# Kernel tuning notes

Measured on AMD Instinct MI355X. Metric: run time of the kernel, lower is better.

Reference implementation:

```python
import jax, jax.numpy as jnp
import numpy as np

NUM_EXPERTS = 8
TOP_K = 2
HIDDEN = 1024
INTER = 4096
BATCH, SEQ = 4, 2048
AUX_COEF = 0.01
Z_COEF = 0.001


def setup_inputs() -> dict:
    key = jax.random.key(0)
    ks = jax.random.split(key, 5)
    scale = 1.0 / np.sqrt(HIDDEN)
    return {
        "hidden_states": jax.random.normal(ks[0], (BATCH, SEQ, HIDDEN), jnp.float32),
        "gate_w": jax.random.normal(ks[1], (NUM_EXPERTS, HIDDEN), jnp.float32) * scale,
        "w_gate": jax.random.normal(ks[2], (NUM_EXPERTS, INTER, HIDDEN), jnp.float32) * scale,
        "w_up": jax.random.normal(ks[3], (NUM_EXPERTS, INTER, HIDDEN), jnp.float32) * scale,
        "w_down": jax.random.normal(ks[4], (NUM_EXPERTS, HIDDEN, INTER), jnp.float32) * (1.0 / np.sqrt(INTER)),
    }


def reference(hidden_states, gate_w, w_gate, w_up, w_down):
    B, S, H = hidden_states.shape
    x = hidden_states.reshape(-1, H)  # [T, H]
    T = x.shape[0]

    # ---- Router ----
    router_logits = x @ gate_w.T                       # [T, E]
    router_probs = jax.nn.softmax(router_logits, axis=-1)
    routing_weights, selected_experts = jax.lax.top_k(router_probs, TOP_K)  # [T, K]
    routing_weights = routing_weights / routing_weights.sum(axis=-1, keepdims=True)

    # ---- Aux losses ----
    expert_mask = jax.nn.one_hot(selected_experts, NUM_EXPERTS, dtype=jnp.float32).sum(axis=1)  # [T, E]
    tokens_per_expert = expert_mask.mean(axis=0)        # [E]
    prob_per_expert = router_probs.mean(axis=0)         # [E]
    load_balancing_loss = NUM_EXPERTS * (tokens_per_expert * prob_per_expert).sum() * AUX_COEF
    router_z_loss = jnp.mean(jax.nn.logsumexp(router_logits, axis=-1) ** 2) * Z_COEF

    # ---- Combine weights: [T, E], zero for unselected experts ----
    combine = (jax.nn.one_hot(selected_experts, NUM_EXPERTS, dtype=x.dtype)
               * routing_weights[..., None]).sum(axis=1)  # [T, E]

    # ---- Expert SwiGLU FFNs, weighted combine (loop over fixed small E) ----
    out = jnp.zeros_like(x)
    for e in range(NUM_EXPERTS):
        h = jax.nn.silu(x @ w_gate[e].T) * (x @ w_up[e].T)  # [T, INTER]
        out = out + combine[:, e:e + 1] * (h @ w_down[e].T)

    return out.reshape(B, S, H), load_balancing_loss, router_z_loss
```

## Files before the change

kernel.cpp:

```cpp
#include <hip/hip_runtime.h>
#include <hip/hip_bf16.h>

#define NUM_TOK 8192
#define HID 1024
#define INT_DIM 4096
#define NEXP 8
#define NSLOT 16384

typedef __bf16 bf16x8 __attribute__((ext_vector_type(8)));
typedef float f32x4 __attribute__((ext_vector_type(4)));

typedef const __attribute__((address_space(1))) unsigned int* gas_t;
typedef __attribute__((address_space(3))) unsigned int* las_t;

__device__ __forceinline__ void gl_lds16(const unsigned short* g, unsigned short* l) {
    __builtin_amdgcn_global_load_lds((gas_t)g, (las_t)l, 16, 0, 0);
}

__device__ __forceinline__ unsigned short f2bf(float f) {
    unsigned int x = __builtin_bit_cast(unsigned int, f);
    x += 0x7fffu + ((x >> 16) & 1u);
    return (unsigned short)(x >> 16);
}

__global__ void k_cvt(const float* __restrict__ src, unsigned short* __restrict__ dst) {
    size_t i = ((size_t)blockIdx.x * 256 + threadIdx.x) * 8;
    float4 a = *(const float4*)(src + i);
    float4 b = *(const float4*)(src + i + 4);
    union { unsigned short us[8]; uint4 v; } o;
    o.us[0] = f2bf(a.x); o.us[1] = f2bf(a.y); o.us[2] = f2bf(a.z); o.us[3] = f2bf(a.w);
    o.us[4] = f2bf(b.x); o.us[5] = f2bf(b.y); o.us[6] = f2bf(b.z); o.us[7] = f2bf(b.w);
    *(uint4*)(dst + i) = o.v;
}

__global__ __launch_bounds__(256) void k_router(
    const float* __restrict__ x, const float* __restrict__ gw,
    int* __restrict__ g_cnt, float* __restrict__ g_prob, float* __restrict__ g_z,
    int* __restrict__ btok, float* __restrict__ bw)
{
    __shared__ float sGw[NEXP * HID];
    __shared__ float sProb[NEXP];
    __shared__ int   sCnt[NEXP];
    __shared__ float sZ;
    __shared__ int   sBase[NEXP];
    __shared__ int   rE0[64], rP0[64], rE1[64], rP1[64];
    __shared__ float rW0[64], rW1[64];

    int tid = threadIdx.x;
    for (int i = tid; i < NEXP * HID; i += 256) sGw[i] = gw[i];
    if (tid < NEXP) { sProb[tid] = 0.f; sCnt[tid] = 0; }
    if (tid == 0) sZ = 0.f;
    __syncthreads();

    int wave = tid >> 6, lane = tid & 63;
    for (int ti = 0; ti < 16; ++ti) {
        int lt = wave * 16 + ti;
        int t = blockIdx.x * 64 + lt;
        const float* xr = x + (size_t)t * HID;
        float acc[NEXP];
        #pragma unroll
        for (int e = 0; e < NEXP; ++e) acc[e] = 0.f;
        for (int k = lane; k < HID; k += 64) {
            float xv = xr[k];
            #pragma unroll
            for (int e = 0; e < NEXP; ++e) acc[e] += xv * sGw[e * HID + k];
        }
        #pragma unroll
        for (int e = 0; e < NEXP; ++e) {
            #pragma unroll
            for (int off = 32; off > 0; off >>= 1)
                acc[e] += __shfl_xor(acc[e], off);
        }
        if (lane == 0) {
            float m = acc[0];
            #pragma unroll
            for (int e = 1; e < NEXP; ++e) m = fmaxf(m, acc[e]);
            float s = 0.f;
            float p[NEXP];
            #pragma unroll
            for (int e = 0; e < NEXP; ++e) { p[e] = __expf(acc[e] - m); s += p[e]; }
            float inv = 1.f / s;
            float v1 = -1e30f, v2 = -1e30f; int i1 = -1, i2 = -1;
            #pragma unroll
            for (int e = 0; e < NEXP; ++e) {
                float v = acc[e];
                if (v > v1) { v2 = v1; i2 = i1; v1 = v; i1 = e; }
                else if (v > v2) { v2 = v; i2 = e; }
            }
            float e1v = __expf(v1 - m), e2v = __expf(v2 - m);
            float w0 = e1v / (e1v + e2v), w1 = e2v / (e1v + e2v);
            float lse = m + __logf(s);
            #pragma unroll
            for (int e = 0; e < NEXP; ++e) atomicAdd(&sProb[e], p[e] * inv);
            atomicAdd(&sZ, lse * lse);
            int p0 = atomicAdd(&sCnt[i1], 1);
            int p1 = atomicAdd(&sCnt[i2], 1);
            rE0[lt] = i1; rP0[lt] = p0; rE1[lt] = i2; rP1[lt] = p1;
            rW0[lt] = w0; rW1[lt] = w1;
        }
    }
    __syncthreads();
    if (tid < NEXP) {
        sBase[tid] = atomicAdd(&g_cnt[tid], sCnt[tid]);
        atomicAdd(&g_prob[tid], sProb[tid]);
    }
    if (tid == 64) atomicAdd(g_z, sZ);
    __syncthreads();
    if (tid < 64) {
        int t = blockIdx.x * 64 + tid;
        int e0 = rE0[tid], e1 = rE1[tid];
        int gp0 = sBase[e0] + rP0[tid];
        int gp1 = sBase[e1] + rP1[tid];
        btok[e0 * NUM_TOK + gp0] = t;
        btok[e1 * NUM_TOK + gp1] = t;
        bw[e0 * NUM_TOK + gp0] = rW0[tid];
        bw[e1 * NUM_TOK + gp1] = rW1[tid];
    }
}

__global__ void k_finalize(const int* __restrict__ g_cnt, const float* __restrict__ g_prob,
                           const float* __restrict__ g_z, int* __restrict__ offs,
                           float* __restrict__ out_tail)
{
    if (threadIdx.x == 0) {
        int o = 0; float lb = 0.f;
        for (int e = 0; e < NEXP; ++e) {
            offs[e] = o; o += g_cnt[e];
            lb += (float)g_cnt[e] * g_prob[e];
        }
        offs[NEXP] = o;
        out_tail[0] = (float)NEXP * lb / ((float)NUM_TOK * (float)NUM_TOK) * 0.01f;
        out_tail[1] = (g_z[0] / (float)NUM_TOK) * 0.001f;
    }
}


#define CFENCE asm volatile("" ::: "memory")
#define BARRF do { CFENCE; __builtin_amdgcn_s_barrier(); CFENCE; } while (0)
#define VMW(n) asm volatile("s_waitcnt vmcnt(" #n ")" ::: "memory")
#define SP1 __builtin_amdgcn_s_setprio(1)
#define SP0 __builtin_amdgcn_s_setprio(0)

#define STG_A(BUF,H,KT) do { \
    gl_lds16(abase + (srcA[(H)*2+0] + (unsigned)(KT)*64u), sm + (BUF)*32768 + (H)*8192 + w*512); \
    gl_lds16(abase + (srcA[(H)*2+1] + (unsigned)(KT)*64u), sm + (BUF)*32768 + (H)*8192 + 4096 + w*512); \
} while (0)
#define STG_B(BUF,N,KT) do { \
    gl_lds16(bbase + (srcB[(N)*2+0] + (unsigned)(KT)*64u), sm + (BUF)*32768 + 16384 + (N)*8192 + w*512); \
    gl_lds16(bbase + (srcB[(N)*2+1] + (unsigned)(KT)*64u), sm + (BUF)*32768 + 16384 + (N)*8192 + 4096 + w*512); \
} while (0)

#define RD_A4(BUF,H,KK) do { \
    const unsigned short* pa_ = sm + (BUF)*32768 + (unsigned)((wm*128 + (H)*64 + l16) * 64); \
    unsigned sw_ = (KK) ? swz1 : swz0; \
    af4[0] = *(const bf16x8*)(pa_ + sw_); \
    af4[1] = *(const bf16x8*)(pa_ + 1024 + sw_); \
    af4[2] = *(const bf16x8*)(pa_ + 2048 + sw_); \
    af4[3] = *(const bf16x8*)(pa_ + 3072 + sw_); \
} while (0)
#define RD_B4(BUF,N,BR) do { \
    const unsigned short* pb_ = sm + (BUF)*32768 + 16384 + (unsigned)(((N)*128 + wn*32 + l16) * 64); \
    BR[0] = *(const bf16x8*)(pb_ + swz0); \
    BR[1] = *(const bf16x8*)(pb_ + swz1); \
    BR[2] = *(const bf16x8*)(pb_ + 1024 + swz0); \
    BR[3] = *(const bf16x8*)(pb_ + 1024 + swz1); \
} while (0)

#define MF8(H,N,BR,KK) do { \
    acc[(H)*4+0][(N)*2+0] = __builtin_amdgcn_mfma_f32_16x16x32_bf16(af4[0], BR[0+(KK)], acc[(H)*4+0][(N)*2+0], 0,0,0); \
    acc[(H)*4+1][(N)*2+0] = __builtin_amdgcn_mfma_f32_16x16x32_bf16(af4[1], BR[0+(KK)], acc[(H)*4+1][(N)*2+0], 0,0,0); \
    acc[(H)*4+2][(N)*2+0] = __builtin_amdgcn_mfma_f32_16x16x32_bf16(af4[2], BR[0+(KK)], acc[(H)*4+2][(N)*2+0], 0,0,0); \
    acc[(H)*4+3][(N)*2+0] = __builtin_amdgcn_mfma_f32_16x16x32_bf16(af4[3], BR[0+(KK)], acc[(H)*4+3][(N)*2+0], 0,0,0); \
    acc[(H)*4+0][(N)*2+1] = __builtin_amdgcn_mfma_f32_16x16x32_bf16(af4[0], BR[2+(KK)], acc[(H)*4+0][(N)*2+1], 0,0,0); \
    acc[(H)*4+1][(N)*2+1] = __builtin_amdgcn_mfma_f32_16x16x32_bf16(af4[1], BR[2+(KK)], acc[(H)*4+1][(N)*2+1], 0,0,0); \
    acc[(H)*4+2][(N)*2+1] = __builtin_amdgcn_mfma_f32_16x16x32_bf16(af4[2], BR[2+(KK)], acc[(H)*4+2][(N)*2+1], 0,0,0); \
    acc[(H)*4+3][(N)*2+1] = __builtin_amdgcn_mfma_f32_16x16x32_bf16(af4[3], BR[2+(KK)], acc[(H)*4+3][(N)*2+1], 0,0,0); \
} while (0)

#define GEMM_MAIN(NTILES) \
    STG_B(0,0,0); STG_B(0,1,0); STG_A(0,0,0); STG_A(0,1,0); \
    STG_B(1,0,1); STG_B(1,1,1); \
    VMW(4); BARRF; \
    _Pragma("unroll 1") \
    for (int T = 0; T < (NTILES); T += 2) { \
        int k1 = T + 1; \
        int k2 = (T + 2 < (NTILES)) ? T + 2 : (NTILES) - 1; \
        int k3 = (T + 3 < (NTILES)) ? T + 3 : (NTILES) - 1; \
         \
        RD_A4(0,0,0); RD_B4(0,0,b0); STG_A(1,0,k1); STG_A(1,1,k1); \
        BARRF; SP1; MF8(0,0,b0,0); RD_A4(0,0,1); MF8(0,0,b0,1); SP0; BARRF; \
         \
        RD_A4(0,0,0); RD_B4(0,1,b1); STG_B(0,0,k2); \
        BARRF; SP1; MF8(0,1,b1,0); RD_A4(0,0,1); MF8(0,1,b1,1); SP0; BARRF; \
         \
        RD_A4(0,1,0); STG_B(0,1,k2); \
        BARRF; SP1; MF8(1,1,b1,0); RD_A4(0,1,1); MF8(1,1,b1,1); SP0; BARRF; \
         \
        RD_A4(0,1,0); \
        BARRF; SP1; MF8(1,0,b0,0); RD_A4(0,1,1); MF8(1,0,b0,1); SP0; VMW(4); BARRF; \
         \
        STG_A(0,0,k2); STG_A(0,1,k2); RD_A4(1,0,0); RD_B4(1,0,b0); \
        BARRF; SP1; MF8(0,0,b0,0); RD_A4(1,0,1); MF8(0,0,b0,1); SP0; BARRF; \
         \
        RD_A4(1,0,0); RD_B4(1,1,b1); STG_B(1,0,k3); \
        BARRF; SP1; MF8(0,1,b1,0); RD_A4(1,0,1); MF8(0,1,b1,1); SP0; BARRF; \
         \
        RD_A4(1,1,0); STG_B(1,1,k3); \
        BARRF; SP1; MF8(1,1,b1,0); RD_A4(1,1,1); MF8(1,1,b1,1); SP0; BARRF; \
         \
        RD_A4(1,1,0); \
        BARRF; SP1; MF8(1,0,b0,0); RD_A4(1,1,1); MF8(1,0,b0,1); SP0; VMW(4); BARRF; \
    } \
    VMW(0);

__global__ __launch_bounds__(512, 2) void k_ffn1(
    const unsigned short* __restrict__ xb, const unsigned short* __restrict__ wgb,
    const unsigned short* __restrict__ wub, unsigned short* __restrict__ hout,
    const int* __restrict__ btok, const int* __restrict__ cnt, const int* __restrict__ offs)
{
    int bswz = (blockIdx.x & 7) * 1024 + (blockIdx.x >> 3);
    int xm = bswz & 255, y = bswz >> 8;
    int e = xm >> 5;
    int mBase = (xm & 31) * 256;
    int ne = cnt[e];
    if (mBase >= ne) return;
    int valid = ne - mBase; if (valid > 256) valid = 256;
    int nBase = y * 128;
    int slotBase = offs[e] + mBase;

    __shared__ alignas(16) unsigned short sm[65536];

    int tid = threadIdx.x;
    int w = tid >> 6, lane = tid & 63;
    int lr = lane >> 3, q = (lane & 7) ^ lr;
    int l16 = lane & 15, quad = lane >> 4;
    int wm = w >> 2, wn = w & 3;

    unsigned swz0 = (unsigned)((quad ^ (l16 & 7)) * 8);
    unsigned swz1 = (unsigned)(((4 + quad) ^ (l16 & 7)) * 8);

    const unsigned short* abase = xb;
    const unsigned short* bbase = wgb;
    unsigned updelta = (unsigned)(size_t)(wub - wgb);

    unsigned srcA[4], srcB[4];
    #pragma unroll
    for (int hh = 0; hh < 2; ++hh)
        #pragma unroll
        for (int t = 0; t < 2; ++t) {
            int row = mBase + hh * 128 + t * 64 + w * 8 + lr;
            if (row > ne - 1) row = ne - 1;
            srcA[hh*2+t] = (unsigned)btok[e * NUM_TOK + row] * (unsigned)HID + (unsigned)(q * 8);
        }
    #pragma unroll
    for (int n = 0; n < 2; ++n)
        #pragma unroll
        for (int t = 0; t < 2; ++t) {
            int r = n * 128 + t * 64 + w * 8 + lr;
            int j = ((r >> 5) << 4) + (r & 15);
            srcB[n*2+t] = ((unsigned)e * INT_DIM + nBase + j) * (unsigned)HID
                        + (((r >> 4) & 1) ? updelta : 0u) + (unsigned)(q * 8);
        }

    f32x4 acc[8][4] = {};
    bf16x8 af4[4], b0[4], b1[4];

    GEMM_MAIN(16)

    #pragma unroll
    for (int hq = 0; hq < 8; ++hq) {
        #pragma unroll
        for (int rr = 0; rr < 4; ++rr) {
            int row = wm * 128 + hq * 16 + quad * 4 + rr;
            if (row < valid) {
                size_t base = (size_t)(slotBase + row) * INT_DIM + nBase;
                #pragma unroll
                for (int n = 0; n < 2; ++n) {
                    float gv = acc[hq][2*n][rr];
                    float uv = acc[hq][2*n+1][rr];
                    float hv = (gv / (1.f + __expf(-gv))) * uv;
                    hout[base + n * 64 + wn * 16 + l16] = f2bf(hv);
                }
            }
        }
    }
}

__global__ __launch_bounds__(512, 2) void k_ffn2(
    const unsigned short* __restrict__ hin, const unsigned short* __restrict__ wdb,
    float* __restrict__ out,
    const int* __restrict__ btok, const float* __restrict__ bw,
    const int* __restrict__ cnt, const int* __restrict__ offs)
{
    int bswz = (blockIdx.x & 7) * 256 + (blockIdx.x >> 3);
    int xm = bswz & 255, yz = bswz >> 8;
    int y = yz & 3, z = yz >> 2;
    int e = xm >> 5;
    int mBase = (xm & 31) * 256;
    int ne = cnt[e];
    if (mBase >= ne) return;
    int valid = ne - mBase; if (valid > 256) valid = 256;
    int nBase = y * 256;
    int kOff = z * (INT_DIM / 2);
    int slotBase = offs[e] + mBase;

    __shared__ alignas(16) unsigned short sm[65536];

    int tid = threadIdx.x;
    int w = tid >> 6, lane = tid & 63;
    int lr = lane >> 3, q = (lane & 7) ^ lr;
    int l16 = lane & 15, quad = lane >> 4;
    int wm = w >> 2, wn = w & 3;

    unsigned swz0 = (unsigned)((quad ^ (l16 & 7)) * 8);
    unsigned swz1 = (unsigned)(((4 + quad) ^ (l16 & 7)) * 8);

    const unsigned short* abase = hin;
    const unsigned short* bbase = wdb;

    unsigned srcA[4], srcB[4];
    #pragma unroll
    for (int hh = 0; hh < 2; ++hh)
        #pragma unroll
        for (int t = 0; t < 2; ++t) {
            int row = hh * 128 + t * 64 + w * 8 + lr;
            if (row > valid - 1) row = valid - 1;
            srcA[hh*2+t] = (unsigned)(slotBase + row) * (unsigned)INT_DIM
                         + (unsigned)kOff + (unsigned)(q * 8);
        }
    #pragma unroll
    for (int n = 0; n < 2; ++n)
        #pragma unroll
        for (int t = 0; t < 2; ++t) {
            int r = n * 128 + t * 64 + w * 8 + lr;
            srcB[n*2+t] = ((unsigned)e * HID + nBase + r) * (unsigned)INT_DIM
                        + (unsigned)kOff + (unsigned)(q * 8);
        }

    f32x4 acc[8][4] = {};
    bf16x8 af4[4], b0[4], b1[4];

    GEMM_MAIN(32)

    #pragma unroll
    for (int hq = 0; hq < 8; ++hq) {
        #pragma unroll
        for (int rr = 0; rr < 4; ++rr) {
            int row = wm * 128 + hq * 16 + quad * 4 + rr;
            if (row < valid) {
                int slot = mBase + row;
                int tok = btok[e * NUM_TOK + slot];
                float wgt = bw[e * NUM_TOK + slot];
                float* ob = out + (size_t)tok * HID + nBase;
                atomicAdd(ob + wn * 32 + l16,             wgt * acc[hq][0][rr]);
                atomicAdd(ob + wn * 32 + 16 + l16,        wgt * acc[hq][1][rr]);
                atomicAdd(ob + 128 + wn * 32 + l16,       wgt * acc[hq][2][rr]);
                atomicAdd(ob + 128 + wn * 32 + 16 + l16,  wgt * acc[hq][3][rr]);
            }
        }
    }
}

extern "C" void kernel_launch(void* const* d_in, const int* in_sizes, int n_in,
                              void* d_out, int out_size, void* d_ws, size_t ws_size,
                              hipStream_t stream) {
    const float* x  = (const float*)d_in[0];
    const float* gw = (const float*)d_in[1];
    const float* wg = (const float*)d_in[2];
    const float* wu = (const float*)d_in[3];
    const float* wd = (const float*)d_in[4];
    float* out = (float*)d_out;

    char* p = (char*)d_ws;
    unsigned short* xb  = (unsigned short*)p; p += (size_t)NUM_TOK * HID * 2;
    unsigned short* h   = (unsigned short*)p; p += (size_t)NSLOT * INT_DIM * 2;
    unsigned short* wgb = (unsigned short*)p; p += (size_t)NEXP * INT_DIM * HID * 2;
    unsigned short* wub = (unsigned short*)p; p += (size_t)NEXP * INT_DIM * HID * 2;
    unsigned short* wdb = (unsigned short*)p; p += (size_t)NEXP * HID * INT_DIM * 2;
    int* btok           = (int*)p;            p += (size_t)NEXP * NUM_TOK * 4;
    float* bw           = (float*)p;          p += (size_t)NEXP * NUM_TOK * 4;
    int* cnt            = (int*)p;            p += 32;
    float* probSum      = (float*)p;          p += 32;
    float* zSum         = (float*)p;          p += 16;
    int* offs           = (int*)p;            p += 64;

    hipMemsetAsync(cnt, 0, 80, stream);
    hipMemsetAsync(out, 0, (size_t)NUM_TOK * HID * sizeof(float), stream);

    k_cvt<<<4096, 256, 0, stream>>>(x, xb);
    k_cvt<<<16384, 256, 0, stream>>>(wg, wgb);
    k_cvt<<<16384, 256, 0, stream>>>(wu, wub);
    k_cvt<<<16384, 256, 0, stream>>>(wd, wdb);
    k_router<<<128, 256, 0, stream>>>(x, gw, cnt, probSum, zSum, btok, bw);
    k_finalize<<<1, 64, 0, stream>>>(cnt, probSum, zSum, offs, out + (size_t)NUM_TOK * HID);
    k_ffn1<<<8192, 512, 0, stream>>>(xb, wgb, wub, h, btok, cnt, offs);
    k_ffn2<<<2048, 512, 0, stream>>>(h, wdb, out, btok, bw, cnt, offs);
}
```

Baseline: 1.084 ms.

## Merge conversion launches, restructure MFMA phases, precompute LDS offsets, remap block grid

```diff
diff --git a/kernel.cpp b/kernel.cpp
--- a/kernel.cpp
+++ b/kernel.cpp
@@ -23,13 +23,24 @@
     return (unsigned short)(x >> 16);
 }
 
-__global__ void k_cvt(const float* __restrict__ src, unsigned short* __restrict__ dst) {
-    size_t i = ((size_t)blockIdx.x * 256 + threadIdx.x) * 8;
+__global__ __launch_bounds__(256) void k_cvtall(
+    const float* __restrict__ x, const float* __restrict__ wg,
+    const float* __restrict__ wu, const float* __restrict__ wd,
+    unsigned short* __restrict__ xb, unsigned short* __restrict__ wgb,
+    unsigned short* __restrict__ wub, unsigned short* __restrict__ wdb)
+{
+    int b = blockIdx.x;
+    const float* src; unsigned short* dst; size_t base;
+    if (b < 4096)       { src = x;  dst = xb;  base = (size_t)b * 2048; }
+    else if (b < 20480) { src = wg; dst = wgb; base = (size_t)(b - 4096) * 2048; }
+    else if (b < 36864) { src = wu; dst = wub; base = (size_t)(b - 20480) * 2048; }
+    else                { src = wd; dst = wdb; base = (size_t)(b - 36864) * 2048; }
+    size_t i = base + (size_t)threadIdx.x * 8;
     float4 a = *(const float4*)(src + i);
-    float4 b = *(const float4*)(src + i + 4);
+    float4 c = *(const float4*)(src + i + 4);
     union { unsigned short us[8]; uint4 v; } o;
     o.us[0] = f2bf(a.x); o.us[1] = f2bf(a.y); o.us[2] = f2bf(a.z); o.us[3] = f2bf(a.w);
-    o.us[4] = f2bf(b.x); o.us[5] = f2bf(b.y); o.us[6] = f2bf(b.z); o.us[7] = f2bf(b.w);
+    o.us[4] = f2bf(c.x); o.us[5] = f2bf(c.y); o.us[6] = f2bf(c.z); o.us[7] = f2bf(c.w);
     *(uint4*)(dst + i) = o.v;
 }
 
@@ -142,39 +153,34 @@
 #define SP0 __builtin_amdgcn_s_setprio(0)
 
 #define STG_A(BUF,H,KT) do { \
-    gl_lds16(abase + (srcA[(H)*2+0] + (unsigned)(KT)*64u), sm + (BUF)*32768 + (H)*8192 + w*512); \
-    gl_lds16(abase + (srcA[(H)*2+1] + (unsigned)(KT)*64u), sm + (BUF)*32768 + (H)*8192 + 4096 + w*512); \
+    gl_lds16(abase + (srcA[(H)*2+0] + (unsigned)(KT)*64u), sm + (BUF)*32768 + (H)*8192 + ldsW); \
+    gl_lds16(abase + (srcA[(H)*2+1] + (unsigned)(KT)*64u), sm + (BUF)*32768 + (H)*8192 + 4096 + ldsW); \
 } while (0)
 #define STG_B(BUF,N,KT) do { \
-    gl_lds16(bbase + (srcB[(N)*2+0] + (unsigned)(KT)*64u), sm + (BUF)*32768 + 16384 + (N)*8192 + w*512); \
-    gl_lds16(bbase + (srcB[(N)*2+1] + (unsigned)(KT)*64u), sm + (BUF)*32768 + 16384 + (N)*8192 + 4096 + w*512); \
+    gl_lds16(bbase + (srcB[(N)*2+0] + (unsigned)(KT)*64u), sm + (BUF)*32768 + 16384 + (N)*8192 + ldsW); \
+    gl_lds16(bbase + (srcB[(N)*2+1] + (unsigned)(KT)*64u), sm + (BUF)*32768 + 16384 + (N)*8192 + 4096 + ldsW); \
 } while (0)
 
 #define RD_A4(BUF,H,KK) do { \
-    const unsigned short* pa_ = sm + (BUF)*32768 + (unsigned)((wm*128 + (H)*64 + l16) * 64); \
-    unsigned sw_ = (KK) ? swz1 : swz0; \
-    af4[0] = *(const bf16x8*)(pa_ + sw_); \
-    af4[1] = *(const bf16x8*)(pa_ + 1024 + sw_); \
-    af4[2] = *(const bf16x8*)(pa_ + 2048 + sw_); \
-    af4[3] = *(const bf16x8*)(pa_ + 3072 + sw_); \
+    unsigned pa_ = (KK) ? oA##BUF##1 : oA##BUF##0; \
+    af4[0] = *(const bf16x8*)(sm + pa_ + (H)*4096);        \
+    af4[1] = *(const bf16x8*)(sm + pa_ + (H)*4096 + 1024); \
+    af4[2] = *(const bf16x8*)(sm + pa_ + (H)*4096 + 2048); \
+    af4[3] = *(const bf16x8*)(sm + pa_ + (H)*4096 + 3072); \
 } while (0)
 #define RD_B4(BUF,N,BR) do { \
-    const unsigned short* pb_ = sm + (BUF)*32768 + 16384 + (unsigned)(((N)*128 + wn*32 + l16) * 64); \
-    BR[0] = *(const bf16x8*)(pb_ + swz0); \
-    BR[1] = *(const bf16x8*)(pb_ + swz1); \
-    BR[2] = *(const bf16x8*)(pb_ + 1024 + swz0); \
-    BR[3] = *(const bf16x8*)(pb_ + 1024 + swz1); \
+    BR[0] = *(const bf16x8*)(sm + oB##BUF##0 + (N)*8192);        \
+    BR[1] = *(const bf16x8*)(sm + oB##BUF##1 + (N)*8192);        \
+    BR[2] = *(const bf16x8*)(sm + oB##BUF##0 + (N)*8192 + 1024); \
+    BR[3] = *(const bf16x8*)(sm + oB##BUF##1 + (N)*8192 + 1024); \
 } while (0)
 
-#define MF8(H,N,BR,KK) do { \
-    acc[(H)*4+0][(N)*2+0] = __builtin_amdgcn_mfma_f32_16x16x32_bf16(af4[0], BR[0+(KK)], acc[(H)*4+0][(N)*2+0], 0,0,0); \
-    acc[(H)*4+1][(N)*2+0] = __builtin_amdgcn_mfma_f32_16x16x32_bf16(af4[1], BR[0+(KK)], acc[(H)*4+1][(N)*2+0], 0,0,0); \
-    acc[(H)*4+2][(N)*2+0] = __builtin_amdgcn_mfma_f32_16x16x32_bf16(af4[2], BR[0+(KK)], acc[(H)*4+2][(N)*2+0], 0,0,0); \
-    acc[(H)*4+3][(N)*2+0] = __builtin_amdgcn_mfma_f32_16x16x32_bf16(af4[3], BR[0+(KK)], acc[(H)*4+3][(N)*2+0], 0,0,0); \
-    acc[(H)*4+0][(N)*2+1] = __builtin_amdgcn_mfma_f32_16x16x32_bf16(af4[0], BR[2+(KK)], acc[(H)*4+0][(N)*2+1], 0,0,0); \
-    acc[(H)*4+1][(N)*2+1] = __builtin_amdgcn_mfma_f32_16x16x32_bf16(af4[1], BR[2+(KK)], acc[(H)*4+1][(N)*2+1], 0,0,0); \
-    acc[(H)*4+2][(N)*2+1] = __builtin_amdgcn_mfma_f32_16x16x32_bf16(af4[2], BR[2+(KK)], acc[(H)*4+2][(N)*2+1], 0,0,0); \
-    acc[(H)*4+3][(N)*2+1] = __builtin_amdgcn_mfma_f32_16x16x32_bf16(af4[3], BR[2+(KK)], acc[(H)*4+3][(N)*2+1], 0,0,0); \
+#define MM(I,N,H,BF) acc[(H)*4+(I)][N] = __builtin_amdgcn_mfma_f32_16x16x32_bf16(af4[I], BF, acc[(H)*4+(I)][N], 0, 0, 0)
+#define MF16(H,KK) do { \
+    MM(0,0,H,b0[KK]);   MM(1,0,H,b0[KK]);   MM(2,0,H,b0[KK]);   MM(3,0,H,b0[KK]);   \
+    MM(0,1,H,b0[2+KK]); MM(1,1,H,b0[2+KK]); MM(2,1,H,b0[2+KK]); MM(3,1,H,b0[2+KK]); \
+    MM(0,2,H,b1[KK]);   MM(1,2,H,b1[KK]);   MM(2,2,H,b1[KK]);   MM(3,2,H,b1[KK]);   \
+    MM(0,3,H,b1[2+KK]); MM(1,3,H,b1[2+KK]); MM(2,3,H,b1[2+KK]); MM(3,3,H,b1[2+KK]); \
 } while (0)
 
 #define GEMM_MAIN(NTILES) \
@@ -187,29 +193,29 @@
         int k2 = (T + 2 < (NTILES)) ? T + 2 : (NTILES) - 1; \
         int k3 = (T + 3 < (NTILES)) ? T + 3 : (NTILES) - 1; \
          \
-        RD_A4(0,0,0); RD_B4(0,0,b0); STG_A(1,0,k1); STG_A(1,1,k1); \
-        BARRF; SP1; MF8(0,0,b0,0); RD_A4(0,0,1); MF8(0,0,b0,1); SP0; BARRF; \
-         \
-        RD_A4(0,0,0); RD_B4(0,1,b1); STG_B(0,0,k2); \
-        BARRF; SP1; MF8(0,1,b1,0); RD_A4(0,0,1); MF8(0,1,b1,1); SP0; BARRF; \
+        RD_A4(0,0,0); RD_B4(0,0,b0); RD_B4(0,1,b1); STG_A(1,0,k1); STG_A(1,1,k1); \
+        BARRF; SP1; MF16(0,0); SP0; BARRF; \
+         \
+        RD_A4(0,0,1); STG_B(0,0,k2); \
+        BARRF; SP1; MF16(0,1); SP0; BARRF; \
          \
         RD_A4(0,1,0); STG_B(0,1,k2); \
-        BARRF; SP1; MF8(1,1,b1,0); RD_A4(0,1,1); MF8(1,1,b1,1); SP0; BARRF; \
-         \
-        RD_A4(0,1,0); \
-        BARRF; SP1; MF8(1,0,b0,0); RD_A4(0,1,1); MF8(1,0,b0,1); SP0; VMW(4); BARRF; \
-         \
-        STG_A(0,0,k2); STG_A(0,1,k2); RD_A4(1,0,0); RD_B4(1,0,b0); \
-        BARRF; SP1; MF8(0,0,b0,0); RD_A4(1,0,1); MF8(0,0,b0,1); SP0; BARRF; \
-         \
-        RD_A4(1,0,0); RD_B4(1,1,b1); STG_B(1,0,k3); \
-        BARRF; SP1; MF8(0,1,b1,0); RD_A4(1,0,1); MF8(0,1,b1,1); SP0; BARRF; \
+        BARRF; SP1; MF16(1,0); SP0; BARRF; \
+         \
+        RD_A4(0,1,1); \
+        BARRF; SP1; MF16(1,1); SP0; VMW(4); BARRF; \
+         \
+        RD_A4(1,0,0); RD_B4(1,0,b0); RD_B4(1,1,b1); STG_A(0,0,k2); STG_A(0,1,k2); \
+        BARRF; SP1; MF16(0,0); SP0; BARRF; \
+         \
+        RD_A4(1,0,1); STG_B(1,0,k3); \
+        BARRF; SP1; MF16(0,1); SP0; BARRF; \
          \
         RD_A4(1,1,0); STG_B(1,1,k3); \
-        BARRF; SP1; MF8(1,1,b1,0); RD_A4(1,1,1); MF8(1,1,b1,1); SP0; BARRF; \
-         \
-        RD_A4(1,1,0); \
-        BARRF; SP1; MF8(1,0,b0,0); RD_A4(1,1,1); MF8(1,0,b0,1); SP0; VMW(4); BARRF; \
+        BARRF; SP1; MF16(1,0); SP0; BARRF; \
+         \
+        RD_A4(1,1,1); \
+        BARRF; SP1; MF16(1,1); SP0; VMW(4); BARRF; \
     } \
     VMW(0);
 
@@ -218,8 +224,12 @@
     const unsigned short* __restrict__ wub, unsigned short* __restrict__ hout,
     const int* __restrict__ btok, const int* __restrict__ cnt, const int* __restrict__ offs)
 {
-    int bswz = (blockIdx.x & 7) * 1024 + (blockIdx.x >> 3);
-    int xm = bswz & 255, y = bswz >> 8;
+    int bid = blockIdx.x;
+    int xcd = bid & 7, local = bid >> 3;
+    int c = xcd * 32 + (local >> 5);
+    int w5 = local & 31;
+    int xm = ((c >> 3) << 3) + (w5 >> 2);
+    int y  = ((c & 7) << 2) + (w5 & 3);
     int e = xm >> 5;
     int mBase = (xm & 31) * 256;
     int ne = cnt[e];
@@ -235,9 +245,16 @@
     int lr = lane >> 3, q = (lane & 7) ^ lr;
     int l16 = lane & 15, quad = lane >> 4;
     int wm = w >> 2, wn = w & 3;
+    unsigned ldsW = (unsigned)(w * 512);
 
     unsigned swz0 = (unsigned)((quad ^ (l16 & 7)) * 8);
     unsigned swz1 = (unsigned)(((4 + quad) ^ (l16 & 7)) * 8);
+    unsigned oA00 = (unsigned)((wm * 128 + l16) * 64) + swz0;
+    unsigned oA01 = (unsigned)((wm * 128 + l16) * 64) + swz1;
+    unsigned oA10 = oA00 + 32768u, oA11 = oA01 + 32768u;
+    unsigned oB00 = 16384u + (unsigned)((wn * 32 + l16) * 64) + swz0;
+    unsigned oB01 = 16384u + (unsigned)((wn * 32 + l16) * 64) + swz1;
+    unsigned oB10 = oB00 + 32768u, oB11 = oB01 + 32768u;
 
     const unsigned short* abase = xb;
     const unsigned short* bbase = wgb;
@@ -292,9 +309,12 @@
     const int* __restrict__ btok, const float* __restrict__ bw,
     const int* __restrict__ cnt, const int* __restrict__ offs)
 {
-    int bswz = (blockIdx.x & 7) * 256 + (blockIdx.x >> 3);
-    int xm = bswz & 255, yz = bswz >> 8;
-    int y = yz & 3, z = yz >> 2;
+    int bid = blockIdx.x;
+    int xcd = bid & 7, local = bid >> 3;
+    int c = xcd * 8 + (local >> 5);
+    int w5 = local & 31;
+    int xm = c * 4 + (w5 >> 3);
+    int y  = w5 & 3, z = (w5 >> 2) & 1;
     int e = xm >> 5;
     int mBase = (xm & 31) * 256;
     int ne = cnt[e];
@@ -311,9 +331,16 @@
     int lr = lane >> 3, q = (lane & 7) ^ lr;
     int l16 = lane & 15, quad = lane >> 4;
     int wm = w >> 2, wn = w & 3;
+    unsigned ldsW = (unsigned)(w * 512);
 
     unsigned swz0 = (unsigned)((quad ^ (l16 & 7)) * 8);
     unsigned swz1 = (unsigned)(((4 + quad) ^ (l16 & 7)) * 8);
+    unsigned oA00 = (unsigned)((wm * 128 + l16) * 64) + swz0;
+    unsigned oA01 = (unsigned)((wm * 128 + l16) * 64) + swz1;
+    unsigned oA10 = oA00 + 32768u, oA11 = oA01 + 32768u;
+    unsigned oB00 = 16384u + (unsigned)((wn * 32 + l16) * 64) + swz0;
+    unsigned oB01 = 16384u + (unsigned)((wn * 32 + l16) * 64) + swz1;
+    unsigned oB10 = oB00 + 32768u, oB11 = oB01 + 32768u;
 
     const unsigned short* abase = hin;
     const unsigned short* bbase = wdb;
@@ -387,10 +414,7 @@
     hipMemsetAsync(cnt, 0, 80, stream);
     hipMemsetAsync(out, 0, (size_t)NUM_TOK * HID * sizeof(float), stream);
 
-    k_cvt<<<4096, 256, 0, stream>>>(x, xb);
-    k_cvt<<<16384, 256, 0, stream>>>(wg, wgb);
-    k_cvt<<<16384, 256, 0, stream>>>(wu, wub);
-    k_cvt<<<16384, 256, 0, stream>>>(wd, wdb);
+    k_cvtall<<<53248, 256, 0, stream>>>(x, wg, wu, wd, xb, wgb, wub, wdb);
     k_router<<<128, 256, 0, stream>>>(x, gw, cnt, probSum, zSum, btok, bw);
     k_finalize<<<1, 64, 0, stream>>>(cnt, probSum, zSum, offs, out + (size_t)NUM_TOK * HID);
     k_ffn1<<<8192, 512, 0, stream>>>(xb, wgb, wub, h, btok, cnt, offs);
```

Result: no change. 1.068 ms (-1.5%).
